# Performance work log

Hardware: AMD Instinct MI355X
Metric: run time of the kernel (lower is better)

The kernel has to match this reference:

```python
import jax, jax.numpy as jnp
import numpy as np

N = 50000      # num nodes
E = 800000     # num edges (before self-loops)
DIN = 256
DOUT = 256
K = 3


def setup_inputs() -> dict:
    key = jax.random.key(0)
    k1, k2, k3 = jax.random.split(key, 3)
    x = jax.random.normal(k1, (N, DIN), dtype=jnp.float32)
    edge_index = jax.random.randint(k2, (2, E), 0, N, dtype=jnp.int32)
    # xavier_uniform for weight [K+1, DIN, DOUT]
    limit = float(np.sqrt(6.0 / (DIN + DOUT)))
    weight = jax.random.uniform(k3, (K + 1, DIN, DOUT), dtype=jnp.float32,
                                minval=-limit, maxval=limit)
    bias = jnp.zeros((DOUT,), dtype=jnp.float32)
    return {"x": x, "edge_index": edge_index, "weight": weight, "bias": bias}


def reference(x, edge_index, weight, bias):
    num_nodes = x.shape[0]
    # add self loops
    loops = jnp.arange(num_nodes, dtype=edge_index.dtype)
    row = jnp.concatenate([edge_index[0], loops])
    col = jnp.concatenate([edge_index[1], loops])
    # degree of row (including self loops)
    deg = jax.ops.segment_sum(jnp.ones_like(row, dtype=x.dtype), row,
                              num_segments=num_nodes)
    deg_inv_sqrt = jnp.where(deg > 0, jax.lax.rsqrt(jnp.maximum(deg, 1e-30)), 0.0)
    # edge-weighted Laplacian values: -D^{-1/2} A D^{-1/2}, +1 on diagonal
    Lvals = -deg_inv_sqrt[row] * deg_inv_sqrt[col]
    Lvals = jnp.where(row == col, Lvals + 1.0, Lvals)

    def spmm(v):  # [N, D] -> [N, D]
        return jax.ops.segment_sum(Lvals[:, None] * v[col], row,
                                   num_segments=num_nodes)

    out = jnp.matmul(x, weight[0])
    Tx_0 = x
    Tx_1 = spmm(x)
    out = out + jnp.matmul(Tx_1, weight[1])
    for k in range(2, K + 1):
        Tx_2 = 2.0 * spmm(Tx_1) - Tx_0
        out = out + jnp.matmul(Tx_2, weight[k])
        Tx_0, Tx_1 = Tx_1, Tx_2
    return out + bias
```

## Files before the change

kernel.cpp:

```cpp
#include <hip/hip_runtime.h>
#include <hip/hip_bf16.h>

#define DFEAT 256

typedef __attribute__((ext_vector_type(8))) short bf16x8;
typedef __attribute__((ext_vector_type(4))) float f32x4;

__device__ __forceinline__ float bf2f(unsigned short u) {
  return __builtin_bit_cast(float, ((unsigned)u) << 16);
}
__device__ __forceinline__ unsigned short f2bf(float f) {
  __hip_bfloat16 h = __float2bfloat16(f);
  return *reinterpret_cast<unsigned short*>(&h);
}
__device__ __forceinline__ void gload_lds16(const void* g, void* l) {
  __builtin_amdgcn_global_load_lds(
      (const __attribute__((address_space(1))) void*)g,
      (__attribute__((address_space(3))) void*)l, 16, 0, 0);
}


__global__ void k_count(const int* __restrict__ ei0, int E, int* __restrict__ cnt) {
  int i = blockIdx.x * blockDim.x + threadIdx.x;
  if (i < E) atomicAdd(&cnt[ei0[i]], 1);
}

__global__ __launch_bounds__(256) void k_scan1(const int* __restrict__ cnt, int N,
                                               int* __restrict__ incl,
                                               int* __restrict__ bsum,
                                               float* __restrict__ dis) {
  __shared__ int sh[256];
  int t = threadIdx.x;
  int i = blockIdx.x * 256 + t;
  int v = (i < N) ? cnt[i] : 0;
  sh[t] = v;
  __syncthreads();
  for (int o = 1; o < 256; o <<= 1) {
    int u = (t >= o) ? sh[t - o] : 0;
    __syncthreads();
    sh[t] += u;
    __syncthreads();
  }
  if (i < N) {
    incl[i] = sh[t];
    dis[i] = rsqrtf((float)(v + 1));
  }
  if (t == 255) bsum[blockIdx.x] = sh[255];
}

__global__ __launch_bounds__(256) void k_scan2(const int* __restrict__ bsum, int nb,
                                               int* __restrict__ boff) {
  __shared__ int sh[256];
  int t = threadIdx.x;
  int v = (t < nb) ? bsum[t] : 0;
  sh[t] = v;
  __syncthreads();
  for (int o = 1; o < 256; o <<= 1) {
    int u = (t >= o) ? sh[t - o] : 0;
    __syncthreads();
    sh[t] += u;
    __syncthreads();
  }
  if (t < nb) boff[t] = sh[t] - v;
}

__global__ __launch_bounds__(256) void k_scan3(const int* __restrict__ cnt,
                                               const int* __restrict__ incl,
                                               const int* __restrict__ boff, int N, int E,
                                               int* __restrict__ rowptr) {
  int i = blockIdx.x * 256 + threadIdx.x;
  if (i < N) rowptr[i] = boff[blockIdx.x] + incl[i] - cnt[i];
  if (i == 0) rowptr[N] = E;
}

__global__ void k_scatter(const int* __restrict__ ei0, const int* __restrict__ ei1, int E,
                          const int* __restrict__ rowptr, int* __restrict__ cursor,
                          const float* __restrict__ dis,
                          int* __restrict__ cols, float* __restrict__ vals) {
  int i = blockIdx.x * blockDim.x + threadIdx.x;
  if (i >= E) return;
  int r = ei0[i];
  int c = ei1[i];
  int pos = rowptr[r] + atomicAdd(&cursor[r], 1);
  cols[pos] = c;
  vals[pos] = -dis[r] * dis[c] + (r == c ? 1.0f : 0.0f);
}


__global__ void k_f2bf(const float* __restrict__ src, unsigned short* __restrict__ dst,
                       int n4) {
  int i = blockIdx.x * blockDim.x + threadIdx.x;
  if (i >= n4) return;
  float4 f = *(const float4*)(src + (size_t)i * 4);
  ushort4 u;
  u.x = f2bf(f.x); u.y = f2bf(f.y); u.z = f2bf(f.z); u.w = f2bf(f.w);
  *(ushort4*)(dst + (size_t)i * 4) = u;
}

__global__ void k_wt(const float* __restrict__ W, unsigned short* __restrict__ WT) {
  int idx = blockIdx.x * 256 + threadIdx.x;
  int n = idx & 255;
  int k = (idx >> 8) & 255;
  int g = idx >> 16;
  WT[(g << 16) | (n << 8) | k] = f2bf(W[idx]);
}


__global__ __launch_bounds__(256) void k_spmm_bf(
    const unsigned short* __restrict__ v, const unsigned short* __restrict__ w,
    unsigned short* __restrict__ y,
    const int* __restrict__ rowptr, const int* __restrict__ cols,
    const float* __restrict__ vals, const float* __restrict__ dis,
    float alpha, float beta) {
  __shared__ float red[3][32][9];
  int r = blockIdx.x;
  int lane = threadIdx.x & 63;
  int w4 = threadIdx.x >> 6;
  int half = lane >> 5;
  int l32 = lane & 31;
  int slot = w4 * 2 + half;
  int fo = l32 * 8;
  float acc[8] = {};
  int e0 = rowptr[r], e1 = rowptr[r + 1];

  int e = e0 + slot;
  for (; e + 8 < e1; e += 16) {
    int cA = cols[e], cB = cols[e + 8];
    float lA = vals[e], lB = vals[e + 8];
    uint4 uA = *(const uint4*)(v + (size_t)cA * DFEAT + fo);
    uint4 uB = *(const uint4*)(v + (size_t)cB * DFEAT + fo);
    const unsigned int* wa = &uA.x;
    const unsigned int* wb = &uB.x;
#pragma unroll
    for (int j = 0; j < 4; ++j) {
      acc[2 * j]     += lA * bf2f(wa[j] & 0xffff) + lB * bf2f(wb[j] & 0xffff);
      acc[2 * j + 1] += lA * bf2f(wa[j] >> 16)    + lB * bf2f(wb[j] >> 16);
    }
  }
  if (e < e1) {
    int c = cols[e];
    float lv = vals[e];
    uint4 u = *(const uint4*)(v + (size_t)c * DFEAT + fo);
    const unsigned int* wu = &u.x;
#pragma unroll
    for (int j = 0; j < 4; ++j) {
      acc[2 * j]     += lv * bf2f(wu[j] & 0xffff);
      acc[2 * j + 1] += lv * bf2f(wu[j] >> 16);
    }
  }

#pragma unroll
  for (int j = 0; j < 8; ++j) acc[j] += __shfl_xor(acc[j], 32);

  if (w4 && !half) {
#pragma unroll
    for (int j = 0; j < 8; ++j) red[w4 - 1][l32][j] = acc[j];
  }
  __syncthreads();
  if (w4 == 0 && !half) {
    float dr = dis[r];
    float sc = 1.0f - dr * dr;
    uint4 uv = *(const uint4*)(v + (size_t)r * DFEAT + fo);
    const unsigned int* vu = &uv.x;
    float wv[8] = {};
    if (beta != 0.0f) {
      uint4 uw = *(const uint4*)(w + (size_t)r * DFEAT + fo);
      const unsigned int* wu = &uw.x;
#pragma unroll
      for (int j = 0; j < 4; ++j) {
        wv[2 * j] = bf2f(wu[j] & 0xffff);
        wv[2 * j + 1] = bf2f(wu[j] >> 16);
      }
    }
    ushort4 o[2];
    unsigned short* op = &o[0].x;
#pragma unroll
    for (int j = 0; j < 8; ++j) {
      float a = acc[j] + red[0][l32][j] + red[1][l32][j] + red[2][l32][j];
      float selfv = (j & 1) ? bf2f(vu[j >> 1] >> 16) : bf2f(vu[j >> 1] & 0xffff);
      a += sc * selfv;
      op[j] = f2bf(alpha * a + beta * wv[j]);
    }
    *(uint4*)(y + (size_t)r * DFEAT + fo) = *(const uint4*)&o[0];
  }
}


__global__ __launch_bounds__(256) void k_gemm4(
    const unsigned short* __restrict__ A0, const unsigned short* __restrict__ A1,
    const unsigned short* __restrict__ A2, const unsigned short* __restrict__ A3,
    const unsigned short* __restrict__ WT,
    const float* __restrict__ bias, float* __restrict__ C, int N) {
  __shared__ __align__(16) unsigned short As[128 * 64];
  __shared__ __align__(16) unsigned short Bs[128 * 64];
  int tid = threadIdx.x;
  int lane = tid & 63;
  int w = tid >> 6;
  int wm = w >> 1, wn = w & 1;
  int brow = blockIdx.x * 128;
  int bcol = blockIdx.y * 128;

  f32x4 acc[4][4] = {};

  int srow = w * 32 + (lane >> 3);
  int skb = ((lane & 7) ^ (lane >> 3)) << 4;

  for (int it = 0; it < 16; ++it) {
    int g = it >> 2;
    int k0 = (it & 3) * 64;
    const unsigned short* Asrc = g == 0 ? A0 : g == 1 ? A1 : g == 2 ? A2 : A3;
    const unsigned short* Bsrc = WT + (g << 16);
    __syncthreads();
#pragma unroll
    for (int c = 0; c < 4; ++c) {
      int r = srow + c * 8;
      int grow = brow + r;
      if (grow >= N) grow = N - 1;
      gload_lds16(Asrc + (size_t)grow * DFEAT + k0 + (skb >> 1),
                  (char*)As + (w * 32 + c * 8) * 128);
      gload_lds16(Bsrc + (size_t)(bcol + r) * DFEAT + k0 + (skb >> 1),
                  (char*)Bs + (w * 32 + c * 8) * 128);
    }
    __syncthreads();
#pragma unroll
    for (int ks = 0; ks < 2; ++ks) {
      bf16x8 af[4], bfr[4];
#pragma unroll
      for (int i = 0; i < 4; ++i) {
        int row = wm * 64 + i * 16 + (lane & 15);
        int kb = (ks * 64 + ((lane >> 4) << 4)) ^ ((row & 7) << 4);
        af[i] = *(const bf16x8*)((const char*)As + row * 128 + kb);
      }
#pragma unroll
      for (int j = 0; j < 4; ++j) {
        int row = wn * 64 + j * 16 + (lane & 15);
        int kb = (ks * 64 + ((lane >> 4) << 4)) ^ ((row & 7) << 4);
        bfr[j] = *(const bf16x8*)((const char*)Bs + row * 128 + kb);
      }
#pragma unroll
      for (int i = 0; i < 4; ++i)
#pragma unroll
        for (int j = 0; j < 4; ++j)
          acc[i][j] = __builtin_amdgcn_mfma_f32_16x16x32_bf16(af[i], bfr[j], acc[i][j], 0, 0, 0);
    }
  }

#pragma unroll
  for (int i = 0; i < 4; ++i) {
    int rowb = brow + wm * 64 + i * 16 + (lane >> 4) * 4;
#pragma unroll
    for (int j = 0; j < 4; ++j) {
      int col = bcol + wn * 64 + j * 16 + (lane & 15);
      float b = bias[col];
#pragma unroll
      for (int q = 0; q < 4; ++q) {
        int r = rowb + q;
        if (r < N) C[(size_t)r * DFEAT + col] = acc[i][j][q] + b;
      }
    }
  }
}


extern "C" void kernel_launch(void* const* d_in, const int* in_sizes, int n_in,
                              void* d_out, int out_size, void* d_ws, size_t ws_size,
                              hipStream_t stream) {
  const float* x = (const float*)d_in[0];
  const int* ei = (const int*)d_in[1];
  const float* weight = (const float*)d_in[2];
  const float* bias = (const float*)d_in[3];
  float* out = (float*)d_out;

  int N = in_sizes[0] / DFEAT;
  int E = in_sizes[1] / 2;
  const int* ei0 = ei;
  const int* ei1 = ei + E;

  char* ws = (char*)d_ws;
  size_t off = 0;
  auto alloc = [&](size_t bytes) {
    void* p = ws + off;
    off = (off + bytes + 255) & ~(size_t)255;
    return p;
  };
  int* cnt = (int*)alloc((size_t)2 * N * sizeof(int));
  int* cursor = cnt + N;
  int* rowptr = (int*)alloc((size_t)(N + 1) * sizeof(int));
  float* dis = (float*)alloc((size_t)N * sizeof(float));
  int* cols = (int*)alloc((size_t)E * sizeof(int));
  float* vals = (float*)alloc((size_t)E * sizeof(float));
  int* incl = (int*)alloc((size_t)N * sizeof(int));
  int* bsum = (int*)alloc(256 * sizeof(int));
  int* boff = (int*)alloc(256 * sizeof(int));
  unsigned short* xbf = (unsigned short*)alloc((size_t)N * DFEAT * 2);
  unsigned short* B1 = (unsigned short*)alloc((size_t)N * DFEAT * 2);
  unsigned short* B2 = (unsigned short*)alloc((size_t)N * DFEAT * 2);
  unsigned short* B3 = (unsigned short*)alloc((size_t)N * DFEAT * 2);
  unsigned short* WT = (unsigned short*)alloc((size_t)4 * DFEAT * DFEAT * 2);

  hipMemsetAsync(cnt, 0, (size_t)2 * N * sizeof(int), stream);

  int eb = (E + 255) / 256;
  int nb = (N + 255) / 256;
  k_count<<<eb, 256, 0, stream>>>(ei0, E, cnt);
  k_scan1<<<nb, 256, 0, stream>>>(cnt, N, incl, bsum, dis);
  k_scan2<<<1, 256, 0, stream>>>(bsum, nb, boff);
  k_scan3<<<nb, 256, 0, stream>>>(cnt, incl, boff, N, E, rowptr);
  k_scatter<<<eb, 256, 0, stream>>>(ei0, ei1, E, rowptr, cursor, dis, cols, vals);

  int n4 = N * DFEAT / 4;
  k_f2bf<<<(n4 + 255) / 256, 256, 0, stream>>>(x, xbf, n4);
  k_wt<<<4 * DFEAT * DFEAT / 256, 256, 0, stream>>>(weight, WT);

  k_spmm_bf<<<N, 256, 0, stream>>>(xbf, xbf, B1, rowptr, cols, vals, dis, 1.0f, 0.0f);
  k_spmm_bf<<<N, 256, 0, stream>>>(B1, xbf, B2, rowptr, cols, vals, dis, 2.0f, -1.0f);
  k_spmm_bf<<<N, 256, 0, stream>>>(B2, B1, B3, rowptr, cols, vals, dis, 2.0f, -1.0f);

  dim3 ggrid((N + 127) / 128, DFEAT / 128);
  k_gemm4<<<ggrid, 256, 0, stream>>>(xbf, B1, B2, B3, WT, bias, out, N);
}
```

Baseline: 358.4 us.

## Split SpMM by feature chunks with per-wave rows and on-the-fly edge weights

Rewrites the SpMM so each block owns a 32-feature chunk (8 chunks) of 16 rows, with each wave handling 4 rows via 4 edge slots × 16 lanes and shuffle reduction, removing the LDS reduction and __syncthreads. Edge weights are now computed on the fly from dis[col] rather than stored, dropping the vals array and its scatter writes. Feature-chunking is meant to make each gathered chunk of v more L2-resident across blocks; the cost is narrower 4-byte loads, repeated reads of cols/dis across 8 chunks, and an extra dis gather per edge.

```diff
diff --git a/kernel.cpp b/kernel.cpp
--- a/kernel.cpp
+++ b/kernel.cpp
@@ -75,15 +75,12 @@
 
 __global__ void k_scatter(const int* __restrict__ ei0, const int* __restrict__ ei1, int E,
                           const int* __restrict__ rowptr, int* __restrict__ cursor,
-                          const float* __restrict__ dis,
-                          int* __restrict__ cols, float* __restrict__ vals) {
+                          int* __restrict__ cols) {
   int i = blockIdx.x * blockDim.x + threadIdx.x;
   if (i >= E) return;
   int r = ei0[i];
-  int c = ei1[i];
   int pos = rowptr[r] + atomicAdd(&cursor[r], 1);
-  cols[pos] = c;
-  vals[pos] = -dis[r] * dis[c] + (r == c ? 1.0f : 0.0f);
+  cols[pos] = ei1[i];
 }
 
 
@@ -106,82 +103,57 @@
 }
 
 
-__global__ __launch_bounds__(256) void k_spmm_bf(
+__global__ __launch_bounds__(256) void k_spmm_ch(
     const unsigned short* __restrict__ v, const unsigned short* __restrict__ w,
     unsigned short* __restrict__ y,
     const int* __restrict__ rowptr, const int* __restrict__ cols,
-    const float* __restrict__ vals, const float* __restrict__ dis,
-    float alpha, float beta) {
-  __shared__ float red[3][32][9];
-  int r = blockIdx.x;
+    const float* __restrict__ dis, float alpha, float beta, int N) {
+  int ch = blockIdx.x & 7;
+  int rbase = (blockIdx.x >> 3) * 16 + (threadIdx.x >> 6) * 4;
   int lane = threadIdx.x & 63;
-  int w4 = threadIdx.x >> 6;
-  int half = lane >> 5;
-  int l32 = lane & 31;
-  int slot = w4 * 2 + half;
-  int fo = l32 * 8;
-  float acc[8] = {};
-  int e0 = rowptr[r], e1 = rowptr[r + 1];
-
-  int e = e0 + slot;
-  for (; e + 8 < e1; e += 16) {
-    int cA = cols[e], cB = cols[e + 8];
-    float lA = vals[e], lB = vals[e + 8];
-    uint4 uA = *(const uint4*)(v + (size_t)cA * DFEAT + fo);
-    uint4 uB = *(const uint4*)(v + (size_t)cB * DFEAT + fo);
-    const unsigned int* wa = &uA.x;
-    const unsigned int* wb = &uB.x;
-#pragma unroll
-    for (int j = 0; j < 4; ++j) {
-      acc[2 * j]     += lA * bf2f(wa[j] & 0xffff) + lB * bf2f(wb[j] & 0xffff);
-      acc[2 * j + 1] += lA * bf2f(wa[j] >> 16)    + lB * bf2f(wb[j] >> 16);
-    }
-  }
-  if (e < e1) {
-    int c = cols[e];
-    float lv = vals[e];
-    uint4 u = *(const uint4*)(v + (size_t)c * DFEAT + fo);
-    const unsigned int* wu = &u.x;
-#pragma unroll
-    for (int j = 0; j < 4; ++j) {
-      acc[2 * j]     += lv * bf2f(wu[j] & 0xffff);
-      acc[2 * j + 1] += lv * bf2f(wu[j] >> 16);
-    }
-  }
-
-#pragma unroll
-  for (int j = 0; j < 8; ++j) acc[j] += __shfl_xor(acc[j], 32);
-
-  if (w4 && !half) {
-#pragma unroll
-    for (int j = 0; j < 8; ++j) red[w4 - 1][l32][j] = acc[j];
-  }
-  __syncthreads();
-  if (w4 == 0 && !half) {
+  int slot = lane >> 4;
+  int fo = ch * 32 + (lane & 15) * 2;
+
+  for (int i = 0; i < 4; ++i) {
+    int r = rbase + i;
+    if (r >= N) return;
+    int e0 = rowptr[r], e1 = rowptr[r + 1];
     float dr = dis[r];
-    float sc = 1.0f - dr * dr;
-    uint4 uv = *(const uint4*)(v + (size_t)r * DFEAT + fo);
-    const unsigned int* vu = &uv.x;
-    float wv[8] = {};
-    if (beta != 0.0f) {
-      uint4 uw = *(const uint4*)(w + (size_t)r * DFEAT + fo);
-      const unsigned int* wu = &uw.x;
-#pragma unroll
-      for (int j = 0; j < 4; ++j) {
-        wv[2 * j] = bf2f(wu[j] & 0xffff);
-        wv[2 * j + 1] = bf2f(wu[j] >> 16);
-      }
-    }
-    ushort4 o[2];
-    unsigned short* op = &o[0].x;
-#pragma unroll
-    for (int j = 0; j < 8; ++j) {
-      float a = acc[j] + red[0][l32][j] + red[1][l32][j] + red[2][l32][j];
-      float selfv = (j & 1) ? bf2f(vu[j >> 1] >> 16) : bf2f(vu[j >> 1] & 0xffff);
-      a += sc * selfv;
-      op[j] = f2bf(alpha * a + beta * wv[j]);
-    }
-    *(uint4*)(y + (size_t)r * DFEAT + fo) = *(const uint4*)&o[0];
+    float a0 = 0.f, a1 = 0.f;
+    int e = e0 + slot;
+    for (; e + 4 < e1; e += 8) {
+      int cA = cols[e], cB = cols[e + 4];
+      float lA = -dr * dis[cA] + (cA == r ? 1.f : 0.f);
+      float lB = -dr * dis[cB] + (cB == r ? 1.f : 0.f);
+      unsigned uA = *(const unsigned*)(v + (size_t)cA * DFEAT + fo);
+      unsigned uB = *(const unsigned*)(v + (size_t)cB * DFEAT + fo);
+      a0 += lA * bf2f(uA & 0xffff) + lB * bf2f(uB & 0xffff);
+      a1 += lA * bf2f(uA >> 16) + lB * bf2f(uB >> 16);
+    }
+    if (e < e1) {
+      int c = cols[e];
+      float lv = -dr * dis[c] + (c == r ? 1.f : 0.f);
+      unsigned u = *(const unsigned*)(v + (size_t)c * DFEAT + fo);
+      a0 += lv * bf2f(u & 0xffff);
+      a1 += lv * bf2f(u >> 16);
+    }
+    a0 += __shfl_xor(a0, 16);
+    a0 += __shfl_xor(a0, 32);
+    a1 += __shfl_xor(a1, 16);
+    a1 += __shfl_xor(a1, 32);
+    if (slot == 0) {
+      float sc = 1.0f - dr * dr;
+      unsigned uv = *(const unsigned*)(v + (size_t)r * DFEAT + fo);
+      float r0 = alpha * (a0 + sc * bf2f(uv & 0xffff));
+      float r1 = alpha * (a1 + sc * bf2f(uv >> 16));
+      if (beta != 0.0f) {
+        unsigned uw = *(const unsigned*)(w + (size_t)r * DFEAT + fo);
+        r0 += beta * bf2f(uw & 0xffff);
+        r1 += beta * bf2f(uw >> 16);
+      }
+      *(unsigned*)(y + (size_t)r * DFEAT + fo) =
+          (unsigned)f2bf(r0) | ((unsigned)f2bf(r1) << 16);
+    }
   }
 }
 
@@ -288,7 +260,6 @@
   int* rowptr = (int*)alloc((size_t)(N + 1) * sizeof(int));
   float* dis = (float*)alloc((size_t)N * sizeof(float));
   int* cols = (int*)alloc((size_t)E * sizeof(int));
-  float* vals = (float*)alloc((size_t)E * sizeof(float));
   int* incl = (int*)alloc((size_t)N * sizeof(int));
   int* bsum = (int*)alloc(256 * sizeof(int));
   int* boff = (int*)alloc(256 * sizeof(int));
@@ -306,15 +277,16 @@
   k_scan1<<<nb, 256, 0, stream>>>(cnt, N, incl, bsum, dis);
   k_scan2<<<1, 256, 0, stream>>>(bsum, nb, boff);
   k_scan3<<<nb, 256, 0, stream>>>(cnt, incl, boff, N, E, rowptr);
-  k_scatter<<<eb, 256, 0, stream>>>(ei0, ei1, E, rowptr, cursor, dis, cols, vals);
+  k_scatter<<<eb, 256, 0, stream>>>(ei0, ei1, E, rowptr, cursor, cols);
 
   int n4 = N * DFEAT / 4;
   k_f2bf<<<(n4 + 255) / 256, 256, 0, stream>>>(x, xbf, n4);
   k_wt<<<4 * DFEAT * DFEAT / 256, 256, 0, stream>>>(weight, WT);
 
-  k_spmm_bf<<<N, 256, 0, stream>>>(xbf, xbf, B1, rowptr, cols, vals, dis, 1.0f, 0.0f);
-  k_spmm_bf<<<N, 256, 0, stream>>>(B1, xbf, B2, rowptr, cols, vals, dis, 2.0f, -1.0f);
-  k_spmm_bf<<<N, 256, 0, stream>>>(B2, B1, B3, rowptr, cols, vals, dis, 2.0f, -1.0f);
+  int sgrid = ((N + 15) / 16) * 8;
+  k_spmm_ch<<<sgrid, 256, 0, stream>>>(xbf, xbf, B1, rowptr, cols, dis, 1.0f, 0.0f, N);
+  k_spmm_ch<<<sgrid, 256, 0, stream>>>(B1, xbf, B2, rowptr, cols, dis, 2.0f, -1.0f, N);
+  k_spmm_ch<<<sgrid, 256, 0, stream>>>(B2, B1, B3, rowptr, cols, dis, 2.0f, -1.0f, N);
 
   dim3 ggrid((N + 127) / 128, DFEAT / 128);
   k_gemm4<<<ggrid, 256, 0, stream>>>(xbf, B1, B2, B3, WT, bias, out, N);
```

New measurement: 639.8 us. 1.79x slower.

## Fold Chebyshev recurrence into weights, compute Laplacian values on the fly, double-buffer GEMM

Applied to the files above, without the earlier changes.

Rewrites the Chebyshev basis as plain Laplacian powers (x, Lx, L²x, L³x) and folds the recurrence coefficients into combined weight matrices. This drops the alpha/beta axpy and the extra previous-term read from each SpMM pass. The edge value array is removed; values are recomputed from the degree array per edge, which saves an E-sized write and read but adds a gather into dis. The GEMM also gains double-buffered LDS staging so the next tile's loads overlap the MFMA work, and a barrier is removed. The reassociated bf16 powers may change numerical error.

```diff
diff --git a/kernel.cpp b/kernel.cpp
--- a/kernel.cpp
+++ b/kernel.cpp
@@ -75,15 +75,12 @@
 
 __global__ void k_scatter(const int* __restrict__ ei0, const int* __restrict__ ei1, int E,
                           const int* __restrict__ rowptr, int* __restrict__ cursor,
-                          const float* __restrict__ dis,
-                          int* __restrict__ cols, float* __restrict__ vals) {
+                          int* __restrict__ cols) {
   int i = blockIdx.x * blockDim.x + threadIdx.x;
   if (i >= E) return;
   int r = ei0[i];
-  int c = ei1[i];
   int pos = rowptr[r] + atomicAdd(&cursor[r], 1);
-  cols[pos] = c;
-  vals[pos] = -dis[r] * dis[c] + (r == c ? 1.0f : 0.0f);
+  cols[pos] = ei1[i];
 }
 
 
@@ -97,21 +94,27 @@
   *(ushort4*)(dst + (size_t)i * 4) = u;
 }
 
-__global__ void k_wt(const float* __restrict__ W, unsigned short* __restrict__ WT) {
+__global__ __launch_bounds__(256) void k_wt(const float* __restrict__ W,
+                                            unsigned short* __restrict__ WT) {
   int idx = blockIdx.x * 256 + threadIdx.x;
   int n = idx & 255;
-  int k = (idx >> 8) & 255;
-  int g = idx >> 16;
-  WT[(g << 16) | (n << 8) | k] = f2bf(W[idx]);
+  int k = idx >> 8;
+  float w0 = W[idx];
+  float w1 = W[65536 + idx];
+  float w2 = W[2 * 65536 + idx];
+  float w3 = W[3 * 65536 + idx];
+  int t = (n << 8) | k;
+  WT[t]               = f2bf(w0 - w2);
+  WT[65536 + t]       = f2bf(w1 - 3.0f * w3);
+  WT[2 * 65536 + t]   = f2bf(2.0f * w2);
+  WT[3 * 65536 + t]   = f2bf(4.0f * w3);
 }
 
 
 __global__ __launch_bounds__(256) void k_spmm_bf(
-    const unsigned short* __restrict__ v, const unsigned short* __restrict__ w,
-    unsigned short* __restrict__ y,
+    const unsigned short* __restrict__ v, unsigned short* __restrict__ y,
     const int* __restrict__ rowptr, const int* __restrict__ cols,
-    const float* __restrict__ vals, const float* __restrict__ dis,
-    float alpha, float beta) {
+    const float* __restrict__ dis) {
   __shared__ float red[3][32][9];
   int r = blockIdx.x;
   int lane = threadIdx.x & 63;
@@ -122,11 +125,13 @@
   int fo = l32 * 8;
   float acc[8] = {};
   int e0 = rowptr[r], e1 = rowptr[r + 1];
+  float dr = dis[r];
 
   int e = e0 + slot;
   for (; e + 8 < e1; e += 16) {
     int cA = cols[e], cB = cols[e + 8];
-    float lA = vals[e], lB = vals[e + 8];
+    float lA = -dr * dis[cA] + (cA == r ? 1.f : 0.f);
+    float lB = -dr * dis[cB] + (cB == r ? 1.f : 0.f);
     uint4 uA = *(const uint4*)(v + (size_t)cA * DFEAT + fo);
     uint4 uB = *(const uint4*)(v + (size_t)cB * DFEAT + fo);
     const unsigned int* wa = &uA.x;
@@ -139,7 +144,7 @@
   }
   if (e < e1) {
     int c = cols[e];
-    float lv = vals[e];
+    float lv = -dr * dis[c] + (c == r ? 1.f : 0.f);
     uint4 u = *(const uint4*)(v + (size_t)c * DFEAT + fo);
     const unsigned int* wu = &u.x;
 #pragma unroll
@@ -158,28 +163,16 @@
   }
   __syncthreads();
   if (w4 == 0 && !half) {
-    float dr = dis[r];
     float sc = 1.0f - dr * dr;
     uint4 uv = *(const uint4*)(v + (size_t)r * DFEAT + fo);
     const unsigned int* vu = &uv.x;
-    float wv[8] = {};
-    if (beta != 0.0f) {
-      uint4 uw = *(const uint4*)(w + (size_t)r * DFEAT + fo);
-      const unsigned int* wu = &uw.x;
-#pragma unroll
-      for (int j = 0; j < 4; ++j) {
-        wv[2 * j] = bf2f(wu[j] & 0xffff);
-        wv[2 * j + 1] = bf2f(wu[j] >> 16);
-      }
-    }
     ushort4 o[2];
     unsigned short* op = &o[0].x;
 #pragma unroll
     for (int j = 0; j < 8; ++j) {
       float a = acc[j] + red[0][l32][j] + red[1][l32][j] + red[2][l32][j];
       float selfv = (j & 1) ? bf2f(vu[j >> 1] >> 16) : bf2f(vu[j >> 1] & 0xffff);
-      a += sc * selfv;
-      op[j] = f2bf(alpha * a + beta * wv[j]);
+      op[j] = f2bf(a + sc * selfv);
     }
     *(uint4*)(y + (size_t)r * DFEAT + fo) = *(const uint4*)&o[0];
   }
@@ -191,8 +184,8 @@
     const unsigned short* __restrict__ A2, const unsigned short* __restrict__ A3,
     const unsigned short* __restrict__ WT,
     const float* __restrict__ bias, float* __restrict__ C, int N) {
-  __shared__ __align__(16) unsigned short As[128 * 64];
-  __shared__ __align__(16) unsigned short Bs[128 * 64];
+  __shared__ __align__(16) unsigned short As[2][128 * 64];
+  __shared__ __align__(16) unsigned short Bs[2][128 * 64];
   int tid = threadIdx.x;
   int lane = tid & 63;
   int w = tid >> 6;
@@ -205,23 +198,29 @@
   int srow = w * 32 + (lane >> 3);
   int skb = ((lane & 7) ^ (lane >> 3)) << 4;
 
-  for (int it = 0; it < 16; ++it) {
+  auto stage = [&](int buf, int it) {
     int g = it >> 2;
     int k0 = (it & 3) * 64;
     const unsigned short* Asrc = g == 0 ? A0 : g == 1 ? A1 : g == 2 ? A2 : A3;
     const unsigned short* Bsrc = WT + (g << 16);
-    __syncthreads();
 #pragma unroll
     for (int c = 0; c < 4; ++c) {
       int r = srow + c * 8;
       int grow = brow + r;
       if (grow >= N) grow = N - 1;
       gload_lds16(Asrc + (size_t)grow * DFEAT + k0 + (skb >> 1),
-                  (char*)As + (w * 32 + c * 8) * 128);
+                  (char*)As[buf] + (w * 32 + c * 8) * 128);
       gload_lds16(Bsrc + (size_t)(bcol + r) * DFEAT + k0 + (skb >> 1),
-                  (char*)Bs + (w * 32 + c * 8) * 128);
-    }
-    __syncthreads();
+                  (char*)Bs[buf] + (w * 32 + c * 8) * 128);
+    }
+  };
+
+  stage(0, 0);
+  __syncthreads();
+
+  for (int it = 0; it < 16; ++it) {
+    int cur = it & 1;
+    if (it < 15) stage(cur ^ 1, it + 1);
 #pragma unroll
     for (int ks = 0; ks < 2; ++ks) {
       bf16x8 af[4], bfr[4];
@@ -229,13 +228,13 @@
       for (int i = 0; i < 4; ++i) {
         int row = wm * 64 + i * 16 + (lane & 15);
         int kb = (ks * 64 + ((lane >> 4) << 4)) ^ ((row & 7) << 4);
-        af[i] = *(const bf16x8*)((const char*)As + row * 128 + kb);
+        af[i] = *(const bf16x8*)((const char*)As[cur] + row * 128 + kb);
       }
 #pragma unroll
       for (int j = 0; j < 4; ++j) {
         int row = wn * 64 + j * 16 + (lane & 15);
         int kb = (ks * 64 + ((lane >> 4) << 4)) ^ ((row & 7) << 4);
-        bfr[j] = *(const bf16x8*)((const char*)Bs + row * 128 + kb);
+        bfr[j] = *(const bf16x8*)((const char*)Bs[cur] + row * 128 + kb);
       }
 #pragma unroll
       for (int i = 0; i < 4; ++i)
@@ -243,6 +242,7 @@
         for (int j = 0; j < 4; ++j)
           acc[i][j] = __builtin_amdgcn_mfma_f32_16x16x32_bf16(af[i], bfr[j], acc[i][j], 0, 0, 0);
     }
+    if (it < 15) __syncthreads();
   }
 
 #pragma unroll
@@ -288,14 +288,13 @@
   int* rowptr = (int*)alloc((size_t)(N + 1) * sizeof(int));
   float* dis = (float*)alloc((size_t)N * sizeof(float));
   int* cols = (int*)alloc((size_t)E * sizeof(int));
-  float* vals = (float*)alloc((size_t)E * sizeof(float));
   int* incl = (int*)alloc((size_t)N * sizeof(int));
   int* bsum = (int*)alloc(256 * sizeof(int));
   int* boff = (int*)alloc(256 * sizeof(int));
   unsigned short* xbf = (unsigned short*)alloc((size_t)N * DFEAT * 2);
-  unsigned short* B1 = (unsigned short*)alloc((size_t)N * DFEAT * 2);
-  unsigned short* B2 = (unsigned short*)alloc((size_t)N * DFEAT * 2);
-  unsigned short* B3 = (unsigned short*)alloc((size_t)N * DFEAT * 2);
+  unsigned short* S1 = (unsigned short*)alloc((size_t)N * DFEAT * 2);
+  unsigned short* S2 = (unsigned short*)alloc((size_t)N * DFEAT * 2);
+  unsigned short* S3 = (unsigned short*)alloc((size_t)N * DFEAT * 2);
   unsigned short* WT = (unsigned short*)alloc((size_t)4 * DFEAT * DFEAT * 2);
 
   hipMemsetAsync(cnt, 0, (size_t)2 * N * sizeof(int), stream);
@@ -306,16 +305,16 @@
   k_scan1<<<nb, 256, 0, stream>>>(cnt, N, incl, bsum, dis);
   k_scan2<<<1, 256, 0, stream>>>(bsum, nb, boff);
   k_scan3<<<nb, 256, 0, stream>>>(cnt, incl, boff, N, E, rowptr);
-  k_scatter<<<eb, 256, 0, stream>>>(ei0, ei1, E, rowptr, cursor, dis, cols, vals);
+  k_scatter<<<eb, 256, 0, stream>>>(ei0, ei1, E, rowptr, cursor, cols);
 
   int n4 = N * DFEAT / 4;
   k_f2bf<<<(n4 + 255) / 256, 256, 0, stream>>>(x, xbf, n4);
-  k_wt<<<4 * DFEAT * DFEAT / 256, 256, 0, stream>>>(weight, WT);
-
-  k_spmm_bf<<<N, 256, 0, stream>>>(xbf, xbf, B1, rowptr, cols, vals, dis, 1.0f, 0.0f);
-  k_spmm_bf<<<N, 256, 0, stream>>>(B1, xbf, B2, rowptr, cols, vals, dis, 2.0f, -1.0f);
-  k_spmm_bf<<<N, 256, 0, stream>>>(B2, B1, B3, rowptr, cols, vals, dis, 2.0f, -1.0f);
+  k_wt<<<DFEAT * DFEAT / 256, 256, 0, stream>>>(weight, WT);
+
+  k_spmm_bf<<<N, 256, 0, stream>>>(xbf, S1, rowptr, cols, dis);
+  k_spmm_bf<<<N, 256, 0, stream>>>(S1, S2, rowptr, cols, dis);
+  k_spmm_bf<<<N, 256, 0, stream>>>(S2, S3, rowptr, cols, dis);
 
   dim3 ggrid((N + 127) / 128, DFEAT / 128);
-  k_gemm4<<<ggrid, 256, 0, stream>>>(xbf, B1, B2, B3, WT, bias, out, N);
-}
+  k_gemm4<<<ggrid, 256, 0, stream>>>(xbf, S1, S2, S3, WT, bias, out, N);
+}
```

After: 360.8 us. No clear change (+0.7%).
